# Optimization experiments

Measured on AMD Instinct MI355X. Metric: run time of the kernel, lower is better.

Reference implementation:

```python
import jax, jax.numpy as jnp
import numpy as np

EMBED_DIM = 1024
B, S = 8, 2048


def setup_inputs() -> dict:
    key = jax.random.key(0)
    ks = jax.random.split(key, 8)
    scale = 1.0 / np.sqrt(EMBED_DIM)
    return {
        "mha_output": jax.random.normal(ks[0], (B, S, EMBED_DIM), dtype=jnp.float32),
        "gates": jax.random.uniform(ks[1], (B, S), dtype=jnp.float32),
        "Wq": jax.random.uniform(ks[2], (EMBED_DIM, EMBED_DIM), jnp.float32, -scale, scale),
        "bq": jax.random.uniform(ks[3], (EMBED_DIM,), jnp.float32, -scale, scale),
        "Wk": jax.random.uniform(ks[4], (EMBED_DIM, EMBED_DIM), jnp.float32, -scale, scale),
        "bk": jax.random.uniform(ks[5], (EMBED_DIM,), jnp.float32, -scale, scale),
        "Wv": jax.random.uniform(ks[6], (EMBED_DIM, EMBED_DIM), jnp.float32, -scale, scale),
        "bv": jax.random.uniform(ks[7], (EMBED_DIM,), jnp.float32, -scale, scale),
    }


def reference(mha_output, gates, Wq, bq, Wk, bk, Wv, bv):
    # gates: (B, S) -> (B, S, 1) for elementwise modulation
    g = gates[..., None]
    # Linear layers (torch convention: x @ W^T + b)
    Q = jnp.einsum('bsd,ed->bse', mha_output, Wq) + bq
    K = jnp.einsum('bsd,ed->bse', mha_output, Wk) + bk
    V = jnp.einsum('bsd,ed->bse', mha_output, Wv) + bv
    Q_mod = Q * g
    K_mod = K * g
    temperature = jnp.sqrt(jnp.asarray(EMBED_DIM, dtype=mha_output.dtype))
    scores = jnp.einsum('bqd,bkd->bqk', Q_mod, K_mod) / temperature  # (B, S, S)
    attn_weights = jax.nn.softmax(scores, axis=-1)
    gated_attn_output = jnp.einsum('bqk,bkd->bqd', attn_weights, V)
    return gated_attn_output, attn_weights
```

## Files before the change

### kernel.cpp

```cpp
#include <hip/hip_runtime.h>

#define SEQ  2048
#define EMB  1024
#define NBAT 8
#define NROW (NBAT*SEQ)

using u16 = unsigned short;
typedef float  f32x4  __attribute__((ext_vector_type(4)));
typedef __bf16 bf16x8 __attribute__((ext_vector_type(8)));
typedef u16    u16x8  __attribute__((ext_vector_type(8)));
typedef u16    u16x4  __attribute__((ext_vector_type(4)));

__device__ __forceinline__ u16 f2bf(float x) {
  unsigned u = __builtin_bit_cast(unsigned, x);
  return (u16)((u + 0x7fffu + ((u >> 16) & 1u)) >> 16);
}
__device__ __forceinline__ float bf2f(u16 h) {
  return __builtin_bit_cast(float, ((unsigned)h) << 16);
}

__device__ __forceinline__ f32x4 mfma16(u16x8 a, u16x8 b, f32x4 c) {
  return __builtin_amdgcn_mfma_f32_16x16x32_bf16(
      __builtin_bit_cast(bf16x8, a), __builtin_bit_cast(bf16x8, b), c, 0, 0, 0);
}

__device__ __forceinline__ void async_cp16(const u16* g, u16* l) {
  __builtin_amdgcn_global_load_lds(
      (const __attribute__((address_space(1))) void*)(g),
      (__attribute__((address_space(3))) void*)(l), 16, 0, 0);
}

__device__ __forceinline__ void stage_half(const u16* __restrict__ g, int ld,
                                           u16* __restrict__ lds, int wid, int lane)
{
  const int lr = lane >> 2;
  const int bb = (lr & 1) ^ ((lr >> 2) & 1);
  const int row16 = (lr & ~1) | bb;
  const int ck = (lane & 3) ^ ((lr & 2) | bb);
#pragma unroll
  for (int l = 0; l < 2; ++l) {
    const int r0 = wid * 32 + l * 16;
    async_cp16(g + (size_t)(r0 + row16) * ld + ck * 8, lds + r0 * 32);
  }
}

__device__ __forceinline__ void ph_reads_A(const u16* __restrict__ sAh, int mg,
                                           int wr, int r, int kg, int xr, u16x8 a[4])
{
#pragma unroll
  for (int i = 0; i < 4; ++i) {
    const int row = wr * 128 + (mg * 4 + i) * 16 + r;
    a[i] = *(const u16x8*)&sAh[(row * 32 + kg * 8) ^ xr];
  }
}
__device__ __forceinline__ void ph_reads_B(const u16* __restrict__ sBh,
                                           int wc, int r, int kg, int xr, u16x8 b[4])
{
#pragma unroll
  for (int j = 0; j < 4; ++j) {
    const int row = wc * 64 + j * 16 + r;
    b[j] = *(const u16x8*)&sBh[(row * 32 + kg * 8) ^ xr];
  }
}

__device__ __forceinline__ void mfma_block(const u16x8 a[4], const u16x8 b[4],
                                           f32x4 (*accp)[4])
{
#pragma unroll
  for (int i = 0; i < 4; ++i)
#pragma unroll
    for (int j = 0; j < 4; ++j)
      accp[i][j] = mfma16(a[i], b[j], accp[i][j]);
}

#define DECL_LDS_8PH()                                                       \
  __shared__ alignas(16) u16 sAls[2][2][256 * 32];                           \
  __shared__ alignas(16) u16 sBls[2][2][256 * 32]

#define PH(READS, STAGE, WAIT, ACCBASE)                                      \
  READS                                                                      \
  STAGE                                                                      \
  WAIT                                                                       \
  __builtin_amdgcn_s_barrier();                                              \
  asm volatile("s_waitcnt lgkmcnt(0)" ::: "memory");                         \
  __builtin_amdgcn_sched_barrier(0);                                         \
  __builtin_amdgcn_s_setprio(1);                                             \
  mfma_block(a_, b_, &acc[ACCBASE]);                                         \
  __builtin_amdgcn_s_setprio(0);                                             \
  __builtin_amdgcn_s_barrier();

#define W_NONE {}
#define W_K1  { if (pf_) asm volatile("s_waitcnt vmcnt(4)" ::: "memory");    \
                else     asm volatile("s_waitcnt vmcnt(0)" ::: "memory");    \
                __builtin_amdgcn_sched_barrier(0); }
#define W_K0N { if (pf_) { asm volatile("s_waitcnt vmcnt(4)" ::: "memory");  \
                __builtin_amdgcn_sched_barrier(0); } }

#define GEMM_8PH(Aptr, ldA, Bptr, ldB, NTv)                                  \
  {                                                                          \
    const int r_ = lane & 15, kg_ = lane >> 4;                               \
    const int xr_ = (r_ & 7) << 3;                                           \
    stage_half((Aptr),      (ldA), &sAls[0][0][0], wid, lane);               \
    stage_half((Bptr),      (ldB), &sBls[0][0][0], wid, lane);               \
    stage_half((Aptr) + 32, (ldA), &sAls[0][1][0], wid, lane);               \
    stage_half((Bptr) + 32, (ldB), &sBls[0][1][0], wid, lane);               \
    asm volatile("s_waitcnt vmcnt(4)" ::: "memory");                         \
    __builtin_amdgcn_sched_barrier(0);                                       \
    __builtin_amdgcn_s_barrier();                                            \
    u16x8 a_[4], b_[4];                                                      \
    for (int tt = 0; tt < (NTv); ++tt) {                                     \
      const int s_ = tt & 1, s2_ = s_ ^ 1;                                   \
      const u16* A0_ = &sAls[s_][0][0]; const u16* A1_ = &sAls[s_][1][0];    \
      const u16* B0_ = &sBls[s_][0][0]; const u16* B1_ = &sBls[s_][1][0];    \
      const bool pf_ = (tt + 1 < (NTv));                                     \
      PH({ ph_reads_A(A0_, 0, wr, r_, kg_, xr_, a_);                         \
           ph_reads_B(B0_, wc, r_, kg_, xr_, b_); },                         \
         { if (pf_) stage_half((Aptr) + (tt + 1) * 64, (ldA),                \
                               &sAls[s2_][0][0], wid, lane); },              \
         W_NONE, 0)                                                          \
      PH({ ph_reads_A(A0_, 1, wr, r_, kg_, xr_, a_); },                      \
         { if (pf_) stage_half((Bptr) + (tt + 1) * 64, (ldB),                \
                               &sBls[s2_][0][0], wid, lane); },              \
         W_K1, 4)                                                            \
      PH({ ph_reads_A(A1_, 0, wr, r_, kg_, xr_, a_);                         \
           ph_reads_B(B1_, wc, r_, kg_, xr_, b_); },                         \
         { if (pf_) stage_half((Aptr) + (tt + 1) * 64 + 32, (ldA),           \
                               &sAls[s2_][1][0], wid, lane); },              \
         W_NONE, 0)                                                          \
      PH({ ph_reads_A(A1_, 1, wr, r_, kg_, xr_, a_); },                      \
         { if (pf_) stage_half((Bptr) + (tt + 1) * 64 + 32, (ldB),           \
                               &sBls[s2_][1][0], wid, lane); },              \
         W_K0N, 4)                                                           \
    }                                                                        \
  }

#define DECL_ACC()                                                           \
  f32x4 acc[8][4];                                                           \
  _Pragma("unroll")                                                          \
  for (int i = 0; i < 8; ++i)                                                \
    _Pragma("unroll")                                                        \
    for (int j = 0; j < 4; ++j)                                              \
      _Pragma("unroll")                                                      \
      for (int q = 0; q < 4; ++q) acc[i][j][q] = 0.0f

__device__ __forceinline__ int xcd_swz(int bid, int nwg) {
  return (bid & 7) * (nwg >> 3) + (bid >> 3);
}

__global__ __launch_bounds__(256) void prep_kernel(
    const float* __restrict__ X,
    const float* __restrict__ Wq, const float* __restrict__ Wk, const float* __restrict__ Wv,
    u16* __restrict__ Xb, u16* __restrict__ Wb)
{
  const size_t i = ((size_t)blockIdx.x * 256 + threadIdx.x) * 4;
  const size_t nx = (size_t)NROW * EMB;
  f32x4 v;
  u16* dst;
  if (i < nx) {
    v = *(const f32x4*)(X + i);
    dst = Xb + i;
  } else {
    const size_t j = i - nx;
    const int m = (int)(j / ((size_t)EMB * EMB));
    const size_t o = j - (size_t)m * EMB * EMB;
    const float* W = (m == 0) ? Wq : (m == 1) ? Wk : Wv;
    v = *(const f32x4*)(W + o);
    dst = Wb + j;
  }
  u16x4 h;
#pragma unroll
  for (int j = 0; j < 4; ++j) h[j] = f2bf(v[j]);
  *(u16x4*)dst = h;
}

__global__ __launch_bounds__(512, 2) void proj_kernel(
    const u16* __restrict__ Xb, const u16* __restrict__ Wb,
    const float* __restrict__ bq, const float* __restrict__ bk, const float* __restrict__ bv,
    u16* __restrict__ Qb, u16* __restrict__ Kb, u16* __restrict__ VT)
{
  DECL_LDS_8PH();
  const int nwg = 4 * 64 * 3;
  int wg = xcd_swz(blockIdx.x, nwg);
  const int n0 = (wg & 3) * 256;        wg >>= 2;
  const int m0 = (wg & 63) * 256;       wg >>= 6;
  const int mat = wg;

  const int t = threadIdx.x, lane = t & 63, wid = t >> 6;
  const int wr = wid >> 2, wc = wid & 3;

  const u16* A = Xb + (size_t)m0 * EMB;
  const u16* B = Wb + (size_t)mat * EMB * EMB + (size_t)n0 * EMB;

  DECL_ACC();
  GEMM_8PH(A, EMB, B, EMB, EMB / 64);

  const float* bias = (mat == 0) ? bq : (mat == 1) ? bk : bv;
  const int r = lane & 15, kg = lane >> 4;
#pragma unroll
  for (int i = 0; i < 8; ++i) {
#pragma unroll
    for (int j = 0; j < 4; ++j) {
      const int c = n0 + wc * 64 + j * 16 + r;
      const float bb = bias[c];
      if (mat == 2) {
        const int bi = m0 >> 11;
        const int sbase = (m0 & (SEQ - 1)) + wr * 128 + i * 16 + kg * 4;
        u16x4 hv;
#pragma unroll
        for (int rg = 0; rg < 4; ++rg) hv[rg] = f2bf(acc[i][j][rg] + bb);
        *(u16x4*)&VT[((size_t)bi * EMB + c) * SEQ + sbase] = hv;
      } else {
        u16* D = (mat == 0) ? Qb : Kb;
#pragma unroll
        for (int rg = 0; rg < 4; ++rg) {
          const int row = m0 + wr * 128 + i * 16 + kg * 4 + rg;
          D[(size_t)row * EMB + c] = f2bf(acc[i][j][rg] + bb);
        }
      }
    }
  }
}

__global__ __launch_bounds__(512, 2) void scores_kernel(
    const u16* __restrict__ Qb, const u16* __restrict__ Kb,
    const float* __restrict__ gates, u16* __restrict__ raw)
{
  DECL_LDS_8PH();
  const int nwg = 8 * 8 * NBAT;
  int wg = xcd_swz(blockIdx.x, nwg);
  const int n0 = (wg & 7) * 256;        wg >>= 3;
  const int q0 = (wg & 7) * 256;        wg >>= 3;
  const int b  = wg;

  const int t = threadIdx.x, lane = t & 63, wid = t >> 6;
  const int wr = wid >> 2, wc = wid & 3;

  const u16* A = Qb + ((size_t)b * SEQ + q0) * EMB;
  const u16* B = Kb + ((size_t)b * SEQ + n0) * EMB;

  DECL_ACC();
  GEMM_8PH(A, EMB, B, EMB, EMB / 64);

  const float* gb = gates + (size_t)b * SEQ;
  u16* rawB = raw + ((size_t)b * SEQ + q0) * SEQ;
  const int r = lane & 15, kg = lane >> 4;

  float gkj[4];
#pragma unroll
  for (int j = 0; j < 4; ++j) gkj[j] = gb[n0 + wc * 64 + j * 16 + r] * 0.03125f;

#pragma unroll
  for (int i = 0; i < 8; ++i) {
#pragma unroll
    for (int rg = 0; rg < 4; ++rg) {
      const int qr = wr * 128 + i * 16 + kg * 4 + rg;
      const float gq = gb[q0 + qr];
#pragma unroll
      for (int j = 0; j < 4; ++j) {
        const int col = n0 + wc * 64 + j * 16 + r;
        rawB[(size_t)qr * SEQ + col] = f2bf(expf(acc[i][j][rg] * gq * gkj[j]));
      }
    }
  }
}

__global__ __launch_bounds__(256) void rownorm_kernel(
    const u16* __restrict__ raw, float* __restrict__ attn, float* __restrict__ invl)
{
  const int row = blockIdx.x;
  const int t = threadIdx.x, lane = t & 63, wid = t >> 6;
  const u16* rp = raw + (size_t)row * SEQ + t * 8;
  u16x8 h = *(const u16x8*)rp;
  float e[8];
  float s = 0.f;
#pragma unroll
  for (int j = 0; j < 8; ++j) { e[j] = bf2f(h[j]); s += e[j]; }
#pragma unroll
  for (int off = 32; off >= 1; off >>= 1) s += __shfl_xor(s, off);
  __shared__ float red[4];
  if (lane == 0) red[wid] = s;
  __syncthreads();
  s = (red[0] + red[1]) + (red[2] + red[3]);
  const float iv = 1.0f / s;
  float* ap = attn + (size_t)row * SEQ + t * 8;
  f32x4 w0, w1;
#pragma unroll
  for (int j = 0; j < 4; ++j) { w0[j] = e[j] * iv; w1[j] = e[j + 4] * iv; }
  *(f32x4*)ap       = w0;
  *(f32x4*)(ap + 4) = w1;
  if (t == 0) invl[row] = iv;
}

__global__ __launch_bounds__(512, 2) void pv_kernel(
    const u16* __restrict__ Eb, const u16* __restrict__ VT,
    const float* __restrict__ invl, float* __restrict__ out)
{
  DECL_LDS_8PH();
  const int nwg = 4 * 8 * NBAT;
  int wg = xcd_swz(blockIdx.x, nwg);
  const int d0 = (wg & 3) * 256;        wg >>= 2;
  const int q0 = (wg & 7) * 256;        wg >>= 3;
  const int b  = wg;

  const int t = threadIdx.x, lane = t & 63, wid = t >> 6;
  const int wr = wid >> 2, wc = wid & 3;

  const u16* A = Eb + ((size_t)b * SEQ + q0) * SEQ;
  const u16* B = VT + ((size_t)b * EMB + d0) * SEQ;

  DECL_ACC();
  GEMM_8PH(A, SEQ, B, SEQ, SEQ / 64);

  const int r = lane & 15, kg = lane >> 4;
#pragma unroll
  for (int i = 0; i < 8; ++i) {
#pragma unroll
    for (int rg = 0; rg < 4; ++rg) {
      const int rowl = q0 + wr * 128 + i * 16 + kg * 4 + rg;
      const float iv = invl[(size_t)b * SEQ + rowl];
#pragma unroll
      for (int j = 0; j < 4; ++j) {
        const int col = d0 + wc * 64 + j * 16 + r;
        out[((size_t)b * SEQ + rowl) * EMB + col] = acc[i][j][rg] * iv;
      }
    }
  }
}

extern "C" void kernel_launch(void* const* d_in, const int* in_sizes, int n_in,
                              void* d_out, int out_size, void* d_ws, size_t ws_size,
                              hipStream_t stream) {
  const float* X  = (const float*)d_in[0];
  const float* g  = (const float*)d_in[1];
  const float* Wq = (const float*)d_in[2];
  const float* bq = (const float*)d_in[3];
  const float* Wk = (const float*)d_in[4];
  const float* bk = (const float*)d_in[5];
  const float* Wv = (const float*)d_in[6];
  const float* bv = (const float*)d_in[7];

  float* out0 = (float*)d_out;
  float* attn = out0 + (size_t)NROW * EMB;

  const size_t rawN = (size_t)NBAT * SEQ * SEQ;
  const size_t need = rawN * 2 + (size_t)NBAT * EMB * SEQ * 2 + (size_t)NROW * 4;
  if (ws_size < need) return;
  u16* region0 = (u16*)d_ws;
  u16* Xb  = region0;
  u16* Wb  = region0 + (size_t)NROW * EMB;
  u16* raw = region0;
  u16* VT  = region0 + rawN;
  float* invl = (float*)(VT + (size_t)NBAT * EMB * SEQ);
  u16* Qb = (u16*)out0;
  u16* Kb = Qb + (size_t)NROW * EMB;

  const int prep_blocks = (int)(((size_t)NROW * EMB + (size_t)3 * EMB * EMB) / 1024);
  prep_kernel   <<<dim3(prep_blocks), 256, 0, stream>>>(X, Wq, Wk, Wv, Xb, Wb);
  proj_kernel   <<<dim3(768), 512, 0, stream>>>(Xb, Wb, bq, bk, bv, Qb, Kb, VT);
  scores_kernel <<<dim3(512), 512, 0, stream>>>(Qb, Kb, g, raw);
  rownorm_kernel<<<dim3(NROW), 256, 0, stream>>>(raw, attn, invl);
  pv_kernel     <<<dim3(256), 512, 0, stream>>>(raw, VT, invl, out0);
}
```

Baseline: 372.8 us.

## Collapse 8-phase GEMM pipeline into 2 phases per K-tile

Restructures the shared GEMM main loop from four phases per 64-wide K tile, each doing 16 MFMAs, to two phases doing 32 MFMAs over all 8 A fragments. All four next-tile async stages are issued together in the first phase, with adjusted vmcnt waits. This halves barrier and waitcnt synchronization per tile and gives longer MFMA bursts. In exchange it needs more registers for A fragments and loses some interleaving of global loads with compute, which could hurt occupancy at launch_bounds(512,2).

```diff
diff --git a/kernel.cpp b/kernel.cpp
--- a/kernel.cpp
+++ b/kernel.cpp
@@ -44,12 +44,12 @@
   }
 }
 
-__device__ __forceinline__ void ph_reads_A(const u16* __restrict__ sAh, int mg,
-                                           int wr, int r, int kg, int xr, u16x8 a[4])
-{
-#pragma unroll
-  for (int i = 0; i < 4; ++i) {
-    const int row = wr * 128 + (mg * 4 + i) * 16 + r;
+__device__ __forceinline__ void ph_reads_A8(const u16* __restrict__ sAh,
+                                            int wr, int r, int kg, int xr, u16x8 a[8])
+{
+#pragma unroll
+  for (int i = 0; i < 8; ++i) {
+    const int row = wr * 128 + i * 16 + r;
     a[i] = *(const u16x8*)&sAh[(row * 32 + kg * 8) ^ xr];
   }
 }
@@ -63,11 +63,11 @@
   }
 }
 
-__device__ __forceinline__ void mfma_block(const u16x8 a[4], const u16x8 b[4],
-                                           f32x4 (*accp)[4])
-{
-#pragma unroll
-  for (int i = 0; i < 4; ++i)
+__device__ __forceinline__ void mfma_block8(const u16x8 a[8], const u16x8 b[4],
+                                            f32x4 (*accp)[4])
+{
+#pragma unroll
+  for (int i = 0; i < 8; ++i)
 #pragma unroll
     for (int j = 0; j < 4; ++j)
       accp[i][j] = mfma16(a[i], b[j], accp[i][j]);
@@ -77,7 +77,7 @@
   __shared__ alignas(16) u16 sAls[2][2][256 * 32];                           \
   __shared__ alignas(16) u16 sBls[2][2][256 * 32]
 
-#define PH(READS, STAGE, WAIT, ACCBASE)                                      \
+#define PH2(READS, STAGE, WAIT)                                              \
   READS                                                                      \
   STAGE                                                                      \
   WAIT                                                                       \
@@ -85,52 +85,47 @@
   asm volatile("s_waitcnt lgkmcnt(0)" ::: "memory");                         \
   __builtin_amdgcn_sched_barrier(0);                                         \
   __builtin_amdgcn_s_setprio(1);                                             \
-  mfma_block(a_, b_, &acc[ACCBASE]);                                         \
+  mfma_block8(a_, b_, acc);                                                  \
   __builtin_amdgcn_s_setprio(0);                                             \
   __builtin_amdgcn_s_barrier();
 
-#define W_NONE {}
-#define W_K1  { if (pf_) asm volatile("s_waitcnt vmcnt(4)" ::: "memory");    \
-                else     asm volatile("s_waitcnt vmcnt(0)" ::: "memory");    \
-                __builtin_amdgcn_sched_barrier(0); }
-#define W_K0N { if (pf_) { asm volatile("s_waitcnt vmcnt(4)" ::: "memory");  \
-                __builtin_amdgcn_sched_barrier(0); } }
-
-#define GEMM_8PH(Aptr, ldA, Bptr, ldB, NTv)                                  \
+#define GEMM_2PH(Aptr, ldA, Bptr, ldB, NTv)                                  \
   {                                                                          \
     const int r_ = lane & 15, kg_ = lane >> 4;                               \
     const int xr_ = (r_ & 7) << 3;                                           \
     stage_half((Aptr),      (ldA), &sAls[0][0][0], wid, lane);               \
+    stage_half((Aptr) + 32, (ldA), &sAls[0][1][0], wid, lane);               \
     stage_half((Bptr),      (ldB), &sBls[0][0][0], wid, lane);               \
-    stage_half((Aptr) + 32, (ldA), &sAls[0][1][0], wid, lane);               \
     stage_half((Bptr) + 32, (ldB), &sBls[0][1][0], wid, lane);               \
-    asm volatile("s_waitcnt vmcnt(4)" ::: "memory");                         \
+    asm volatile("s_waitcnt vmcnt(2)" ::: "memory");                         \
     __builtin_amdgcn_sched_barrier(0);                                       \
     __builtin_amdgcn_s_barrier();                                            \
-    u16x8 a_[4], b_[4];                                                      \
+    u16x8 a_[8], b_[4];                                                      \
     for (int tt = 0; tt < (NTv); ++tt) {                                     \
       const int s_ = tt & 1, s2_ = s_ ^ 1;                                   \
       const u16* A0_ = &sAls[s_][0][0]; const u16* A1_ = &sAls[s_][1][0];    \
       const u16* B0_ = &sBls[s_][0][0]; const u16* B1_ = &sBls[s_][1][0];    \
       const bool pf_ = (tt + 1 < (NTv));                                     \
-      PH({ ph_reads_A(A0_, 0, wr, r_, kg_, xr_, a_);                         \
-           ph_reads_B(B0_, wc, r_, kg_, xr_, b_); },                         \
-         { if (pf_) stage_half((Aptr) + (tt + 1) * 64, (ldA),                \
-                               &sAls[s2_][0][0], wid, lane); },              \
-         W_NONE, 0)                                                          \
-      PH({ ph_reads_A(A0_, 1, wr, r_, kg_, xr_, a_); },                      \
-         { if (pf_) stage_half((Bptr) + (tt + 1) * 64, (ldB),                \
-                               &sBls[s2_][0][0], wid, lane); },              \
-         W_K1, 4)                                                            \
-      PH({ ph_reads_A(A1_, 0, wr, r_, kg_, xr_, a_);                         \
-           ph_reads_B(B1_, wc, r_, kg_, xr_, b_); },                         \
-         { if (pf_) stage_half((Aptr) + (tt + 1) * 64 + 32, (ldA),           \
-                               &sAls[s2_][1][0], wid, lane); },              \
-         W_NONE, 0)                                                          \
-      PH({ ph_reads_A(A1_, 1, wr, r_, kg_, xr_, a_); },                      \
-         { if (pf_) stage_half((Bptr) + (tt + 1) * 64 + 32, (ldB),           \
-                               &sBls[s2_][1][0], wid, lane); },              \
-         W_K0N, 4)                                                           \
+      PH2({ ph_reads_A8(A0_, wr, r_, kg_, xr_, a_);                          \
+            ph_reads_B(B0_, wc, r_, kg_, xr_, b_); },                        \
+          { if (pf_) {                                                       \
+              stage_half((Aptr) + (tt + 1) * 64,      (ldA),                 \
+                         &sAls[s2_][0][0], wid, lane);                       \
+              stage_half((Aptr) + (tt + 1) * 64 + 32, (ldA),                 \
+                         &sAls[s2_][1][0], wid, lane);                       \
+              stage_half((Bptr) + (tt + 1) * 64,      (ldB),                 \
+                         &sBls[s2_][0][0], wid, lane);                       \
+              stage_half((Bptr) + (tt + 1) * 64 + 32, (ldB),                 \
+                         &sBls[s2_][1][0], wid, lane);                       \
+            } },                                                             \
+          { if (pf_) asm volatile("s_waitcnt vmcnt(8)" ::: "memory");        \
+            else     asm volatile("s_waitcnt vmcnt(0)" ::: "memory");        \
+            __builtin_amdgcn_sched_barrier(0); })                            \
+      PH2({ ph_reads_A8(A1_, wr, r_, kg_, xr_, a_);                          \
+            ph_reads_B(B1_, wc, r_, kg_, xr_, b_); },                        \
+          { },                                                               \
+          { if (pf_) { asm volatile("s_waitcnt vmcnt(2)" ::: "memory");      \
+            __builtin_amdgcn_sched_barrier(0); } })                          \
     }                                                                        \
   }
 
@@ -192,7 +187,7 @@
   const u16* B = Wb + (size_t)mat * EMB * EMB + (size_t)n0 * EMB;
 
   DECL_ACC();
-  GEMM_8PH(A, EMB, B, EMB, EMB / 64);
+  GEMM_2PH(A, EMB, B, EMB, EMB / 64);
 
   const float* bias = (mat == 0) ? bq : (mat == 1) ? bk : bv;
   const int r = lane & 15, kg = lane >> 4;
@@ -239,7 +234,7 @@
   const u16* B = Kb + ((size_t)b * SEQ + n0) * EMB;
 
   DECL_ACC();
-  GEMM_8PH(A, EMB, B, EMB, EMB / 64);
+  GEMM_2PH(A, EMB, B, EMB, EMB / 64);
 
   const float* gb = gates + (size_t)b * SEQ;
   u16* rawB = raw + ((size_t)b * SEQ + q0) * SEQ;
@@ -309,7 +304,7 @@
   const u16* B = VT + ((size_t)b * EMB + d0) * SEQ;
 
   DECL_ACC();
-  GEMM_8PH(A, SEQ, B, SEQ, SEQ / 64);
+  GEMM_2PH(A, SEQ, B, SEQ, SEQ / 64);
 
   const int r = lane & 15, kg = lane >> 4;
 #pragma unroll
```

After: 349.3 us. 6.3% less time.
